# Kernel optimization log

Measured on AMD Instinct MI355X. Metric: run time of the kernel, lower is better.

The kernel has to match this reference:

```python
import jax, jax.numpy as jnp
import numpy as np

B, L, D, K = 16, 2048, 768, 32
NEG = jnp.float32(-1e30)

def setup_inputs() -> dict:
    key = jax.random.key(0)
    k1, k2, k3, k4 = jax.random.split(key, 4)
    token_hidden = jax.random.normal(k1, (B, L, D), dtype=jnp.float32)
    attention_mask = jnp.ones((B, L), dtype=jnp.float32)
    # ragged spans: sorted boundaries -> contiguous, possibly-empty spans
    bounds = jnp.sort(jax.random.randint(k2, (B, K + 1), 0, L), axis=-1)
    span_starts = bounds[:, :-1].astype(jnp.int32)   # [B, K]
    span_ends = bounds[:, 1:].astype(jnp.int32)      # [B, K]
    w_pool = jax.random.normal(k3, (D,), dtype=jnp.float32) * 0.02
    b_pool = jax.random.normal(k4, (1,), dtype=jnp.float32) * 0.02
    return {"token_hidden": token_hidden, "attention_mask": attention_mask,
            "span_starts": span_starts, "span_ends": span_ends,
            "w_pool": w_pool, "b_pool": b_pool}

def reference(token_hidden, attention_mask, span_starts, span_ends, w_pool, b_pool):
    # sent_pool(vecs): scores per token, shared across spans  -> [B, L]
    scores = jnp.einsum('bld,d->bl', token_hidden, w_pool) + b_pool[0]
    pos = jnp.arange(token_hidden.shape[1], dtype=jnp.int32)  # [L]
    # span membership mask [B, K, L]; empty / out-of-range spans -> all False
    span_mask = ((pos[None, None, :] >= span_starts[:, :, None]) &
                 (pos[None, None, :] < span_ends[:, :, None]) &
                 (attention_mask[:, None, :] >= 0.5))
    logits = jnp.where(span_mask, scores[:, None, :], NEG)  # [B, K, L]
    m = jnp.max(logits, axis=-1, keepdims=True)
    e = jnp.exp(logits - m) * span_mask                      # stable masked softmax
    s = jnp.sum(e, axis=-1, keepdims=True)
    w = e / jnp.maximum(s, jnp.float32(1e-30))               # zero rows for empty spans
    H = jnp.einsum('bkl,bld->bkd', w, token_hidden)          # [B, K, D]
    sent_mask = jnp.any(span_mask, axis=-1).astype(jnp.float32)  # [B, K]
    return H, sent_mask
```

## Files before the change

kernel.cpp:

```cpp
#include <hip/hip_runtime.h>

#define BB 16
#define LL 2048
#define DD 768
#define KK 32
#define NEGI -1e30f
#define NW 16

__global__ __launch_bounds__(1024) void span_pool_k(
    const float* __restrict__ th,
    const float* __restrict__ attn,
    const int* __restrict__ sps,
    const int* __restrict__ spe,
    const float* __restrict__ wp,
    float* __restrict__ Hout,
    float* __restrict__ sent) {
  const int bk = blockIdx.x;
  const int b = bk >> 5;
  const int lane = threadIdx.x & 63;
  const int wave = threadIdx.x >> 6;

  __shared__ float sacc[NW][DD];
  __shared__ float sm[NW], ssm[NW];

  int s0 = min(max(sps[bk], 0), LL);
  int e0 = min(max(spe[bk], 0), LL);

  const float4* wr = (const float4*)wp;
  const float4 w0 = wr[lane], w1 = wr[lane + 64], w2 = wr[lane + 128];

  const float* arow = attn + (size_t)b * LL;
  const float4* tb = (const float4*)(th + (size_t)b * LL * DD);

  float m = NEGI, s = 0.f;
  float4 a0 = make_float4(0.f, 0.f, 0.f, 0.f), a1 = a0, a2 = a0;

  #pragma unroll 2
  for (int l = s0 + wave; l < e0; l += NW) {
    const float4* row = tb + (size_t)l * (DD / 4);
    float4 r0 = row[lane], r1 = row[lane + 64], r2 = row[lane + 128];
    float am = arow[l];

    float d = 0.f;
    d = fmaf(r0.x, w0.x, d); d = fmaf(r0.y, w0.y, d);
    d = fmaf(r0.z, w0.z, d); d = fmaf(r0.w, w0.w, d);
    d = fmaf(r1.x, w1.x, d); d = fmaf(r1.y, w1.y, d);
    d = fmaf(r1.z, w1.z, d); d = fmaf(r1.w, w1.w, d);
    d = fmaf(r2.x, w2.x, d); d = fmaf(r2.y, w2.y, d);
    d = fmaf(r2.z, w2.z, d); d = fmaf(r2.w, w2.w, d);
    #pragma unroll
    for (int o = 32; o > 0; o >>= 1) d += __shfl_xor(d, o, 64);

    if (am >= 0.5f) {
      const float nm = fmaxf(m, d);
      const float sc = __expf(m - nm);
      const float e  = __expf(d - nm);
      s = fmaf(s, sc, e);
      a0.x = fmaf(e, r0.x, a0.x * sc); a0.y = fmaf(e, r0.y, a0.y * sc);
      a0.z = fmaf(e, r0.z, a0.z * sc); a0.w = fmaf(e, r0.w, a0.w * sc);
      a1.x = fmaf(e, r1.x, a1.x * sc); a1.y = fmaf(e, r1.y, a1.y * sc);
      a1.z = fmaf(e, r1.z, a1.z * sc); a1.w = fmaf(e, r1.w, a1.w * sc);
      a2.x = fmaf(e, r2.x, a2.x * sc); a2.y = fmaf(e, r2.y, a2.y * sc);
      a2.z = fmaf(e, r2.z, a2.z * sc); a2.w = fmaf(e, r2.w, a2.w * sc);
      m = nm;
    }
  }

  float4* sa = (float4*)sacc[wave];
  sa[lane] = a0; sa[lane + 64] = a1; sa[lane + 128] = a2;
  if (lane == 0) { sm[wave] = m; ssm[wave] = s; }
  __syncthreads();

  const int t = threadIdx.x;
  if (t < DD / 4) {
    float M = NEGI;
    #pragma unroll
    for (int w = 0; w < NW; ++w) M = fmaxf(M, sm[w]);
    float S = 0.f;
    #pragma unroll
    for (int w = 0; w < NW; ++w) S = fmaf(__expf(sm[w] - M), ssm[w], S);
    const float inv = (S > 0.f) ? (1.0f / S) : 0.f;

    float4 o = make_float4(0.f, 0.f, 0.f, 0.f);
    #pragma unroll
    for (int w = 0; w < NW; ++w) {
      const float ew = __expf(sm[w] - M);
      const float4 p = ((const float4*)sacc[w])[t];
      o.x = fmaf(ew, p.x, o.x); o.y = fmaf(ew, p.y, o.y);
      o.z = fmaf(ew, p.z, o.z); o.w = fmaf(ew, p.w, o.w);
    }
    o.x *= inv; o.y *= inv; o.z *= inv; o.w *= inv;
    ((float4*)(Hout + (size_t)bk * DD))[t] = o;
    if (t == 0) sent[bk] = (S > 0.f) ? 1.0f : 0.0f;
  }
}

extern "C" void kernel_launch(void* const* d_in, const int* in_sizes, int n_in,
                              void* d_out, int out_size, void* d_ws, size_t ws_size,
                              hipStream_t stream) {
  const float* th   = (const float*)d_in[0];
  const float* attn = (const float*)d_in[1];
  const int*   sps  = (const int*)d_in[2];
  const int*   spe  = (const int*)d_in[3];
  const float* wp   = (const float*)d_in[4];

  float* Hout = (float*)d_out;
  float* sent = Hout + (size_t)BB * KK * DD;

  span_pool_k<<<dim3(BB * KK), dim3(1024), 0, stream>>>(
      th, attn, sps, spe, wp, Hout, sent);
}
```

Before: 167.9 us.

## Split each span across multiple blocks with a second kernel to merge partials

```diff
diff --git a/kernel.cpp b/kernel.cpp
--- a/kernel.cpp
+++ b/kernel.cpp
@@ -5,23 +5,28 @@
 #define DD 768
 #define KK 32
 #define NEGI -1e30f
-#define NW 16
+#define JJ 8
+#define AW 4
+#define SLOTS (JJ * AW)
 
-__global__ __launch_bounds__(1024) void span_pool_k(
+__global__ __launch_bounds__(256) void span_pool_a(
     const float* __restrict__ th,
     const float* __restrict__ attn,
     const int* __restrict__ sps,
     const int* __restrict__ spe,
     const float* __restrict__ wp,
-    float* __restrict__ Hout,
-    float* __restrict__ sent) {
+    float* __restrict__ pacc,
+    float* __restrict__ pm,
+    float* __restrict__ ps) {
   const int bk = blockIdx.x;
-  const int b = bk >> 5;
+  const int j  = blockIdx.y;
+  const int b  = bk >> 5;
   const int lane = threadIdx.x & 63;
   const int wave = threadIdx.x >> 6;
+  const int slot = j * AW + wave;
 
-  __shared__ float sacc[NW][DD];
-  __shared__ float sm[NW], ssm[NW];
+  __shared__ float sacc[AW][DD];
+  __shared__ float sm[AW], ss[AW];
 
   int s0 = min(max(sps[bk], 0), LL);
   int e0 = min(max(spe[bk], 0), LL);
@@ -36,7 +41,7 @@
   float4 a0 = make_float4(0.f, 0.f, 0.f, 0.f), a1 = a0, a2 = a0;
 
   #pragma unroll 2
-  for (int l = s0 + wave; l < e0; l += NW) {
+  for (int l = s0 + slot; l < e0; l += SLOTS) {
     const float4* row = tb + (size_t)l * (DD / 4);
     float4 r0 = row[lane], r1 = row[lane + 64], r2 = row[lane + 128];
     float am = arow[l];
@@ -68,31 +73,62 @@
 
   float4* sa = (float4*)sacc[wave];
   sa[lane] = a0; sa[lane + 64] = a1; sa[lane + 128] = a2;
-  if (lane == 0) { sm[wave] = m; ssm[wave] = s; }
+  if (lane == 0) { sm[wave] = m; ss[wave] = s; }
   __syncthreads();
 
   const int t = threadIdx.x;
   if (t < DD / 4) {
     float M = NEGI;
     #pragma unroll
-    for (int w = 0; w < NW; ++w) M = fmaxf(M, sm[w]);
+    for (int w = 0; w < AW; ++w) M = fmaxf(M, sm[w]);
     float S = 0.f;
-    #pragma unroll
-    for (int w = 0; w < NW; ++w) S = fmaf(__expf(sm[w] - M), ssm[w], S);
-    const float inv = (S > 0.f) ? (1.0f / S) : 0.f;
-
     float4 o = make_float4(0.f, 0.f, 0.f, 0.f);
     #pragma unroll
-    for (int w = 0; w < NW; ++w) {
+    for (int w = 0; w < AW; ++w) {
       const float ew = __expf(sm[w] - M);
+      S = fmaf(ew, ss[w], S);
       const float4 p = ((const float4*)sacc[w])[t];
       o.x = fmaf(ew, p.x, o.x); o.y = fmaf(ew, p.y, o.y);
       o.z = fmaf(ew, p.z, o.z); o.w = fmaf(ew, p.w, o.w);
     }
-    o.x *= inv; o.y *= inv; o.z *= inv; o.w *= inv;
-    ((float4*)(Hout + (size_t)bk * DD))[t] = o;
-    if (t == 0) sent[bk] = (S > 0.f) ? 1.0f : 0.0f;
+    ((float4*)(pacc + (size_t)(bk * JJ + j) * DD))[t] = o;
+    if (t == 0) { pm[bk * JJ + j] = M; ps[bk * JJ + j] = S; }
   }
+}
+
+__global__ __launch_bounds__(192) void span_pool_b(
+    const float* __restrict__ pacc,
+    const float* __restrict__ pm,
+    const float* __restrict__ ps,
+    float* __restrict__ Hout,
+    float* __restrict__ sent) {
+  const int bk = blockIdx.x;
+  const int t = threadIdx.x;
+
+  float mj[JJ], sj[JJ];
+  float M = NEGI;
+  #pragma unroll
+  for (int jv = 0; jv < JJ; ++jv) {
+    mj[jv] = pm[bk * JJ + jv];
+    sj[jv] = ps[bk * JJ + jv];
+    M = fmaxf(M, mj[jv]);
+  }
+  float S = 0.f;
+  #pragma unroll
+  for (int jv = 0; jv < JJ; ++jv) S = fmaf(__expf(mj[jv] - M), sj[jv], S);
+  const float inv = (S > 0.f) ? (1.0f / S) : 0.f;
+
+  float4 o = make_float4(0.f, 0.f, 0.f, 0.f);
+  #pragma unroll
+  for (int jv = 0; jv < JJ; ++jv) {
+    const float ew = __expf(mj[jv] - M);
+    const float4 p = ((const float4*)(pacc + (size_t)(bk * JJ + jv) * DD))[t];
+    o.x = fmaf(ew, p.x, o.x); o.y = fmaf(ew, p.y, o.y);
+    o.z = fmaf(ew, p.z, o.z); o.w = fmaf(ew, p.w, o.w);
+  }
+  o.x *= inv; o.y *= inv; o.z *= inv; o.w *= inv;
+  ((float4*)(Hout + (size_t)bk * DD))[t] = o;
+  if (t == 0) sent[bk] = (S > 0.f) ? 1.0f : 0.0f;
 }
 
 extern "C" void kernel_launch(void* const* d_in, const int* in_sizes, int n_in,
@@ -107,6 +143,12 @@
   float* Hout = (float*)d_out;
   float* sent = Hout + (size_t)BB * KK * DD;
 
-  span_pool_k<<<dim3(BB * KK), dim3(1024), 0, stream>>>(
-      th, attn, sps, spe, wp, Hout, sent);
+  float* pacc = (float*)d_ws;
+  float* pm   = pacc + (size_t)BB * KK * JJ * DD;
+  float* ps   = pm + (size_t)BB * KK * JJ;
+
+  span_pool_a<<<dim3(BB * KK, JJ), dim3(256), 0, stream>>>(
+      th, attn, sps, spe, wp, pacc, pm, ps);
+  span_pool_b<<<dim3(BB * KK), dim3(192), 0, stream>>>(
+      pacc, pm, ps, Hout, sent);
 }
```

Measured after the change: 167.1 us. About the same (-0.5%).
